# Kernel optimization log

Hardware: AMD Instinct MI355X
Metric: run time of the kernel (lower is better)

The kernel has to match this reference:

```python
import jax, jax.numpy as jnp
import numpy as np

TEMPERATURE = 1.0
EPS = 1e-12  # matches torch F.normalize default eps


def setup_inputs() -> dict:
    key = jax.random.key(0)
    k1, k2 = jax.random.split(key)
    B, N, D = 8, 2048, 768
    final_features = jax.random.normal(k1, (B, N, D), dtype=jnp.float32)
    mid_features = jax.random.normal(k2, (B, N, D), dtype=jnp.float32)
    return {"final_features": final_features, "mid_features": mid_features}


def reference(final_features, mid_features):
    B, N, D = final_features.shape
    dtype = final_features.dtype

    mid = mid_features.astype(jnp.float32)
    # L2-normalize along feature dim (torch F.normalize: x / max(||x||, eps))
    norm = jnp.maximum(jnp.linalg.norm(mid, axis=-1, keepdims=True), EPS)
    mid_n = mid / norm

    # [B, N, N] cosine similarity
    sim = jnp.einsum("bnd,bmd->bnm", mid_n, mid_n)
    # zero out diagonal (add_self_similarity=False): sim * (1 - eye)
    eye = jnp.eye(N, dtype=sim.dtype)
    sim = sim * (1.0 - eye)[None, :, :]

    # confidence = row-wise max of (zeroed-diagonal) similarity
    confidence = jnp.max(sim, axis=-1)  # [B, N]

    # softmax over scaled similarities (diagonal entries are exactly 0, kept in softmax)
    weights = jax.nn.softmax(sim / TEMPERATURE, axis=-1)  # [B, N, N]

    refined = jnp.einsum("bnm,bmd->bnd", weights, final_features.astype(jnp.float32))

    cw = confidence[..., None].astype(dtype)  # [B, N, 1]
    calibrated = cw * refined.astype(dtype) + (1.0 - cw) * final_features
    return calibrated
```

## Files before the change

kernel.cpp:

```cpp
#include <hip/hip_runtime.h>
#include <hip/hip_bf16.h>

static constexpr int BB = 8;
static constexpr int NN = 2048;
static constexpr int DD = 768;

typedef __attribute__((ext_vector_type(8))) __bf16 bf16x8;
typedef __attribute__((ext_vector_type(4))) float f32x4;

__device__ __forceinline__ void gload_lds16(const __hip_bfloat16* g, __hip_bfloat16* l) {
  __builtin_amdgcn_global_load_lds(
      (const __attribute__((address_space(1))) void*)g,
      (__attribute__((address_space(3))) void*)l,
      16, 0, 0);
}

static constexpr int NORM_BLOCKS = (BB * NN) / 4;
static constexpr int TRANS_BLOCKS = (DD / 32) * (NN / 32) * BB;
__global__ void prep_kernel(const float* __restrict__ mid, __hip_bfloat16* __restrict__ Qn,
                            float* __restrict__ lsum, float* __restrict__ conf,
                            const float* __restrict__ F, __hip_bfloat16* __restrict__ Vt) {
  __shared__ __hip_bfloat16 tile[32][33];
  const int t = threadIdx.x;
  if (blockIdx.x < NORM_BLOCKS) {
    const int wave = t >> 6;
    const int lane = t & 63;
    const size_t row = (size_t)blockIdx.x * 4 + wave;
    if (lane == 0) { lsum[row] = 0.f; conf[row] = 0.f; }
    const float* src = mid + row * DD;

    float4 v[3];
    float ss = 0.f;
#pragma unroll
    for (int j = 0; j < 3; ++j) {
      v[j] = *(const float4*)(src + j * 256 + lane * 4);
      ss += v[j].x * v[j].x + v[j].y * v[j].y + v[j].z * v[j].z + v[j].w * v[j].w;
    }
#pragma unroll
    for (int o = 32; o; o >>= 1) ss += __shfl_xor(ss, o, 64);
    const float inv = 1.0f / fmaxf(sqrtf(ss), 1e-12f);

    __hip_bfloat16* dst = Qn + row * DD;
#pragma unroll
    for (int j = 0; j < 3; ++j) {
      union { ushort4 u; __hip_bfloat16 h[4]; } pk;
      pk.h[0] = __float2bfloat16(v[j].x * inv);
      pk.h[1] = __float2bfloat16(v[j].y * inv);
      pk.h[2] = __float2bfloat16(v[j].z * inv);
      pk.h[3] = __float2bfloat16(v[j].w * inv);
      *(ushort4*)(dst + j * 256 + lane * 4) = pk.u;
    }
  } else {
    const int bid = blockIdx.x - NORM_BLOCKS;
    const int bx = bid % 24;
    const int rest = bid / 24;
    const int by = rest & 63;
    const int b = rest >> 6;
    const int n0 = by * 32;
    const int d0 = bx * 32;
    const int tx = t & 31, ty = t >> 5;
#pragma unroll
    for (int i = 0; i < 4; ++i) {
      const int n = n0 + ty + i * 8;
      tile[ty + i * 8][tx] = __float2bfloat16(F[((size_t)b * NN + n) * DD + d0 + tx]);
    }
    __syncthreads();
#pragma unroll
    for (int i = 0; i < 4; ++i) {
      const int d = d0 + ty + i * 8;
      Vt[((size_t)b * DD + d) * NN + n0 + tx] = tile[tx][ty + i * 8];
    }
  }
}

__global__ __launch_bounds__(256) void gemm_qk_kernel(
    const __hip_bfloat16* __restrict__ Qn,
    __hip_bfloat16* __restrict__ P,
    float* __restrict__ lsum,
    unsigned* __restrict__ conf) {
  __shared__ __hip_bfloat16 smem[4 * 128 * 64];

  const int d = blockIdx.x;
  const int b = d & 7;
  int rem = d >> 3;
  int ti = 0;
  while (rem >= 16 - ti) { rem -= 16 - ti; ++ti; }
  const int tj = ti + rem;
  const int rowBase = ti * 128;
  const int colBase = tj * 128;
  const bool offdiag = (ti != tj);

  const int t = threadIdx.x;
  const int lane = t & 63;
  const int wave = t >> 6;
  const int wRow = wave >> 1;
  const int wCol = wave & 1;
  const int quad = lane >> 4;
  const int l16 = lane & 15;

  const __hip_bfloat16* Abase = Qn + ((size_t)b * NN + rowBase) * DD;
  const __hip_bfloat16* Bbase = Qn + ((size_t)b * NN + colBase) * DD;

  int srow[4], scol[4], sc8[4];
#pragma unroll
  for (int i = 0; i < 4; ++i) {
    const int c = i * 256 + t;
    srow[i] = c >> 3;
    const int col8 = (c & 7) ^ ((c >> 3) & 7);
    scol[i] = col8 * 8;
    sc8[i] = c * 8;
  }

  f32x4 acc[4][4];
#pragma unroll
  for (int i = 0; i < 4; ++i)
#pragma unroll
    for (int j = 0; j < 4; ++j) acc[i][j] = (f32x4){0.f, 0.f, 0.f, 0.f};

  {
    __hip_bfloat16* As = smem;
    __hip_bfloat16* Bs = smem + 128 * 64;
#pragma unroll
    for (int i = 0; i < 4; ++i) {
      gload_lds16(Abase + (size_t)srow[i] * DD + scol[i], As + sc8[i]);
      gload_lds16(Bbase + (size_t)srow[i] * DD + scol[i], Bs + sc8[i]);
    }
  }

  constexpr int NK = DD / 64;
  for (int kk = 0; kk < NK; ++kk) {
    const int cur = kk & 1;
    __syncthreads();
    if (kk + 1 < NK) {
      __hip_bfloat16* As = smem + (1 - cur) * 2 * 128 * 64;
      __hip_bfloat16* Bs = As + 128 * 64;
      const int k0 = (kk + 1) * 64;
#pragma unroll
      for (int i = 0; i < 4; ++i) {
        gload_lds16(Abase + (size_t)srow[i] * DD + (k0 + scol[i]), As + sc8[i]);
        gload_lds16(Bbase + (size_t)srow[i] * DD + (k0 + scol[i]), Bs + sc8[i]);
      }
    }
    const __hip_bfloat16* As = smem + cur * 2 * 128 * 64;
    const __hip_bfloat16* Bs = As + 128 * 64;
#pragma unroll
    for (int ks = 0; ks < 2; ++ks) {
      bf16x8 af[4], bfr[4];
#pragma unroll
      for (int i = 0; i < 4; ++i) {
        const int rA = wRow * 64 + i * 16 + l16;
        const int rB = wCol * 64 + i * 16 + l16;
        const int pA = (ks * 4 + quad) ^ (rA & 7);
        const int pB = (ks * 4 + quad) ^ (rB & 7);
        af[i]  = *(const bf16x8*)(As + rA * 64 + pA * 8);
        bfr[i] = *(const bf16x8*)(Bs + rB * 64 + pB * 8);
      }
#pragma unroll
      for (int mi = 0; mi < 4; ++mi)
#pragma unroll
        for (int ni = 0; ni < 4; ++ni)
          acc[mi][ni] = __builtin_amdgcn_mfma_f32_16x16x32_bf16(af[mi], bfr[ni], acc[mi][ni], 0, 0, 0);
    }
  }

  __syncthreads();
  __hip_bfloat16* Pt = smem;
  __hip_bfloat16* Mt = smem + 128 * 128;

  float csum[4] = {0.f, 0.f, 0.f, 0.f};
  float cmax[4] = {0.f, 0.f, 0.f, 0.f};

#pragma unroll
  for (int mi = 0; mi < 4; ++mi) {
    const int rbase = wRow * 64 + mi * 16 + quad * 4;
    float rs[4] = {0.f, 0.f, 0.f, 0.f};
    float rm[4] = {0.f, 0.f, 0.f, 0.f};
#pragma unroll
    for (int ni = 0; ni < 4; ++ni) {
      const int colL = wCol * 64 + ni * 16 + l16;
      const int col_g = colBase + colL;
      union { ushort4 u; __hip_bfloat16 h[4]; } pk;
#pragma unroll
      for (int r = 0; r < 4; ++r) {
        const int rowL = rbase + r;
        float s = acc[mi][ni][r];
        if (rowBase + rowL == col_g) s = 0.f;
        const float p = __expf(s);
        rm[r] = fmaxf(rm[r], s);
        rs[r] += p;
        csum[ni] += p;
        cmax[ni] = fmaxf(cmax[ni], s);
        pk.h[r] = __float2bfloat16(p);
        Pt[rowL * 128 + (((colL >> 3) ^ (rowL & 7)) << 3) + (colL & 7)] = pk.h[r];
      }
      if (offdiag) {
        *(ushort4*)(Mt + colL * 128 + (((rbase >> 3) ^ (colL & 7)) << 3) + (rbase & 7)) = pk.u;
      }
    }
#pragma unroll
    for (int r = 0; r < 4; ++r) {
      float ps = rs[r], mx = rm[r];
#pragma unroll
      for (int o = 1; o < 16; o <<= 1) {
        ps += __shfl_xor(ps, o, 64);
        mx = fmaxf(mx, __shfl_xor(mx, o, 64));
      }
      if (l16 == 0) {
        const int row_g = rowBase + rbase + r;
        atomicAdd(lsum + (size_t)b * NN + row_g, ps);
        atomicMax(conf + (size_t)b * NN + row_g, __float_as_uint(mx));
      }
    }
  }

  if (offdiag) {
#pragma unroll
    for (int ni = 0; ni < 4; ++ni) {
      float cs = csum[ni];
      float cm = cmax[ni];
      cs += __shfl_xor(cs, 16, 64); cm = fmaxf(cm, __shfl_xor(cm, 16, 64));
      cs += __shfl_xor(cs, 32, 64); cm = fmaxf(cm, __shfl_xor(cm, 32, 64));
      if (quad == 0) {
        const int col_g = colBase + wCol * 64 + ni * 16 + l16;
        atomicAdd(lsum + (size_t)b * NN + col_g, cs);
        atomicMax(conf + (size_t)b * NN + col_g, __float_as_uint(cm));
      }
    }
  }

  __syncthreads();
  {
    const size_t pBase = ((size_t)b * NN + rowBase) * (size_t)NN + colBase;
#pragma unroll
    for (int i = 0; i < 8; ++i) {
      const int c = i * 256 + t;
      const int row = c >> 4;
      const int ck = c & 15;
      *(uint4*)(P + pBase + (size_t)row * NN + ck * 8) =
          *(const uint4*)(Pt + row * 128 + ((ck ^ (row & 7)) << 3));
    }
  }
  if (offdiag) {
    const size_t pBase = ((size_t)b * NN + colBase) * (size_t)NN + rowBase;
#pragma unroll
    for (int i = 0; i < 8; ++i) {
      const int c = i * 256 + t;
      const int row = c >> 4;
      const int ck = c & 15;
      *(uint4*)(P + pBase + (size_t)row * NN + ck * 8) =
          *(const uint4*)(Mt + row * 128 + ((ck ^ (row & 7)) << 3));
    }
  }
}

__global__ __launch_bounds__(256) void gemm_pv_kernel(
    const __hip_bfloat16* __restrict__ P,
    const __hip_bfloat16* __restrict__ Vt,
    const float* __restrict__ lsum,
    const float* __restrict__ conf,
    const float* __restrict__ F,
    float* __restrict__ Out) {
  __shared__ __hip_bfloat16 smem[4 * 128 * 64];

  const int d = blockIdx.x;
  const int work = (d & 7) * 96 + (d >> 3);
  const int colBase = (work % 6) * 128;
  const int rowBase = ((work / 6) & 15) * 128;
  const int b = work / 96;

  const int t = threadIdx.x;
  const int lane = t & 63;
  const int wave = t >> 6;
  const int wRow = wave >> 1;
  const int wCol = wave & 1;
  const int quad = lane >> 4;
  const int l16 = lane & 15;

  const __hip_bfloat16* Abase = P + (size_t)b * NN * NN + (size_t)rowBase * NN;
  const __hip_bfloat16* Bbase = Vt + (size_t)b * DD * NN + (size_t)colBase * NN;

  int srow[4], scol[4], sc8[4];
#pragma unroll
  for (int i = 0; i < 4; ++i) {
    const int c = i * 256 + t;
    srow[i] = c >> 3;
    const int col8 = (c & 7) ^ ((c >> 3) & 7);
    scol[i] = col8 * 8;
    sc8[i] = c * 8;
  }

  f32x4 acc[4][4];
#pragma unroll
  for (int i = 0; i < 4; ++i)
#pragma unroll
    for (int j = 0; j < 4; ++j) acc[i][j] = (f32x4){0.f, 0.f, 0.f, 0.f};

  {
    __hip_bfloat16* As = smem;
    __hip_bfloat16* Bs = smem + 128 * 64;
#pragma unroll
    for (int i = 0; i < 4; ++i) {
      gload_lds16(Abase + (size_t)srow[i] * NN + scol[i], As + sc8[i]);
      gload_lds16(Bbase + (size_t)srow[i] * NN + scol[i], Bs + sc8[i]);
    }
  }

  constexpr int NK = NN / 64;
  for (int kk = 0; kk < NK; ++kk) {
    const int cur = kk & 1;
    __syncthreads();
    if (kk + 1 < NK) {
      __hip_bfloat16* As = smem + (1 - cur) * 2 * 128 * 64;
      __hip_bfloat16* Bs = As + 128 * 64;
      const int k0 = (kk + 1) * 64;
#pragma unroll
      for (int i = 0; i < 4; ++i) {
        gload_lds16(Abase + (size_t)srow[i] * NN + (k0 + scol[i]), As + sc8[i]);
        gload_lds16(Bbase + (size_t)srow[i] * NN + (k0 + scol[i]), Bs + sc8[i]);
      }
    }
    const __hip_bfloat16* As = smem + cur * 2 * 128 * 64;
    const __hip_bfloat16* Bs = As + 128 * 64;
#pragma unroll
    for (int ks = 0; ks < 2; ++ks) {
      bf16x8 af[4], bfr[4];
#pragma unroll
      for (int i = 0; i < 4; ++i) {
        const int rA = wRow * 64 + i * 16 + l16;
        const int rB = wCol * 64 + i * 16 + l16;
        const int pA = (ks * 4 + quad) ^ (rA & 7);
        const int pB = (ks * 4 + quad) ^ (rB & 7);
        af[i]  = *(const bf16x8*)(As + rA * 64 + pA * 8);
        bfr[i] = *(const bf16x8*)(Bs + rB * 64 + pB * 8);
      }
#pragma unroll
      for (int mi = 0; mi < 4; ++mi)
#pragma unroll
        for (int ni = 0; ni < 4; ++ni)
          acc[mi][ni] = __builtin_amdgcn_mfma_f32_16x16x32_bf16(af[mi], bfr[ni], acc[mi][ni], 0, 0, 0);
    }
  }

#pragma unroll
  for (int mi = 0; mi < 4; ++mi) {
#pragma unroll
    for (int r = 0; r < 4; ++r) {
      const int row_g = rowBase + wRow * 64 + mi * 16 + quad * 4 + r;
      const float li = lsum[(size_t)b * NN + row_g];
      const float cw = conf[(size_t)b * NN + row_g];
      const float inv = 1.0f / li;
      const float* frow = F + ((size_t)b * NN + row_g) * DD;
      float* orow = Out + ((size_t)b * NN + row_g) * DD;
#pragma unroll
      for (int ni = 0; ni < 4; ++ni) {
        const int col_g = colBase + wCol * 64 + ni * 16 + l16;
        const float o = acc[mi][ni][r] * inv;
        orow[col_g] = cw * o + (1.f - cw) * frow[col_g];
      }
    }
  }
}

extern "C" void kernel_launch(void* const* d_in, const int* in_sizes, int n_in,
                              void* d_out, int out_size, void* d_ws, size_t ws_size,
                              hipStream_t stream) {
  const float* F = (const float*)d_in[0];
  const float* M = (const float*)d_in[1];
  float* Out = (float*)d_out;

  char* ws = (char*)d_ws;
  __hip_bfloat16* Qn = (__hip_bfloat16*)(ws);
  __hip_bfloat16* Vt = (__hip_bfloat16*)(ws + 25165824);
  __hip_bfloat16* P  = (__hip_bfloat16*)(ws + 50331648);
  float* lsum        = (float*)(ws + 117440512);
  float* conf        = (float*)(ws + 117506048);

  prep_kernel<<<NORM_BLOCKS + TRANS_BLOCKS, 256, 0, stream>>>(M, Qn, lsum, conf, F, Vt);
  gemm_qk_kernel<<<8 * 136, 256, 0, stream>>>(Qn, P, lsum, (unsigned*)conf);
  gemm_pv_kernel<<<768, 256, 0, stream>>>(P, Vt, lsum, conf, F, Out);
}
```

Before: 266.5 us.

## Move V transpose into QK launch, reorder tiles, widen PV tiles to 128x192

The F-to-bf16 transpose into Vt moves out of the prep kernel and into the QK GEMM launch as extra tail blocks, so it runs alongside the GEMM tiles instead of before them. QK tile enumeration now schedules the off-diagonal tiles first and the diagonal tiles last. The PV GEMM uses 128x192 output tiles with 6 MFMA columns per wave, giving 512 blocks instead of 768. The wider tile cuts redundant re-reads of P but uses more LDS and accumulator registers, which may lower occupancy.

```diff
diff --git a/kernel.cpp b/kernel.cpp
--- a/kernel.cpp
+++ b/kernel.cpp
@@ -17,41 +17,53 @@
 
 static constexpr int NORM_BLOCKS = (BB * NN) / 4;
 static constexpr int TRANS_BLOCKS = (DD / 32) * (NN / 32) * BB;
+static constexpr int QK_BLOCKS = BB * 136;
+
 __global__ void prep_kernel(const float* __restrict__ mid, __hip_bfloat16* __restrict__ Qn,
-                            float* __restrict__ lsum, float* __restrict__ conf,
-                            const float* __restrict__ F, __hip_bfloat16* __restrict__ Vt) {
-  __shared__ __hip_bfloat16 tile[32][33];
+                            float* __restrict__ lsum, float* __restrict__ conf) {
   const int t = threadIdx.x;
-  if (blockIdx.x < NORM_BLOCKS) {
-    const int wave = t >> 6;
-    const int lane = t & 63;
-    const size_t row = (size_t)blockIdx.x * 4 + wave;
-    if (lane == 0) { lsum[row] = 0.f; conf[row] = 0.f; }
-    const float* src = mid + row * DD;
-
-    float4 v[3];
-    float ss = 0.f;
-#pragma unroll
-    for (int j = 0; j < 3; ++j) {
-      v[j] = *(const float4*)(src + j * 256 + lane * 4);
-      ss += v[j].x * v[j].x + v[j].y * v[j].y + v[j].z * v[j].z + v[j].w * v[j].w;
-    }
-#pragma unroll
-    for (int o = 32; o; o >>= 1) ss += __shfl_xor(ss, o, 64);
-    const float inv = 1.0f / fmaxf(sqrtf(ss), 1e-12f);
-
-    __hip_bfloat16* dst = Qn + row * DD;
-#pragma unroll
-    for (int j = 0; j < 3; ++j) {
-      union { ushort4 u; __hip_bfloat16 h[4]; } pk;
-      pk.h[0] = __float2bfloat16(v[j].x * inv);
-      pk.h[1] = __float2bfloat16(v[j].y * inv);
-      pk.h[2] = __float2bfloat16(v[j].z * inv);
-      pk.h[3] = __float2bfloat16(v[j].w * inv);
-      *(ushort4*)(dst + j * 256 + lane * 4) = pk.u;
-    }
-  } else {
-    const int bid = blockIdx.x - NORM_BLOCKS;
+  const int wave = t >> 6;
+  const int lane = t & 63;
+  const size_t row = (size_t)blockIdx.x * 4 + wave;
+  if (lane == 0) { lsum[row] = 0.f; conf[row] = 0.f; }
+  const float* src = mid + row * DD;
+
+  float4 v[3];
+  float ss = 0.f;
+#pragma unroll
+  for (int j = 0; j < 3; ++j) {
+    v[j] = *(const float4*)(src + j * 256 + lane * 4);
+    ss += v[j].x * v[j].x + v[j].y * v[j].y + v[j].z * v[j].z + v[j].w * v[j].w;
+  }
+#pragma unroll
+  for (int o = 32; o; o >>= 1) ss += __shfl_xor(ss, o, 64);
+  const float inv = 1.0f / fmaxf(sqrtf(ss), 1e-12f);
+
+  __hip_bfloat16* dst = Qn + row * DD;
+#pragma unroll
+  for (int j = 0; j < 3; ++j) {
+    union { ushort4 u; __hip_bfloat16 h[4]; } pk;
+    pk.h[0] = __float2bfloat16(v[j].x * inv);
+    pk.h[1] = __float2bfloat16(v[j].y * inv);
+    pk.h[2] = __float2bfloat16(v[j].z * inv);
+    pk.h[3] = __float2bfloat16(v[j].w * inv);
+    *(ushort4*)(dst + j * 256 + lane * 4) = pk.u;
+  }
+}
+
+__global__ __launch_bounds__(256) void gemm_qk_kernel(
+    const __hip_bfloat16* __restrict__ Qn,
+    __hip_bfloat16* __restrict__ P,
+    float* __restrict__ lsum,
+    unsigned* __restrict__ conf,
+    const float* __restrict__ F,
+    __hip_bfloat16* __restrict__ Vt) {
+  __shared__ __hip_bfloat16 smem[4 * 128 * 64];
+  const int t = threadIdx.x;
+
+  if (blockIdx.x >= QK_BLOCKS) {
+    __hip_bfloat16 (*tile)[33] = reinterpret_cast<__hip_bfloat16(*)[33]>(smem);
+    const int bid = blockIdx.x - QK_BLOCKS;
     const int bx = bid % 24;
     const int rest = bid / 24;
     const int by = rest & 63;
@@ -70,27 +82,24 @@
       const int d = d0 + ty + i * 8;
       Vt[((size_t)b * DD + d) * NN + n0 + tx] = tile[tx][ty + i * 8];
     }
-  }
-}
-
-__global__ __launch_bounds__(256) void gemm_qk_kernel(
-    const __hip_bfloat16* __restrict__ Qn,
-    __hip_bfloat16* __restrict__ P,
-    float* __restrict__ lsum,
-    unsigned* __restrict__ conf) {
-  __shared__ __hip_bfloat16 smem[4 * 128 * 64];
+    return;
+  }
 
   const int d = blockIdx.x;
   const int b = d & 7;
   int rem = d >> 3;
-  int ti = 0;
-  while (rem >= 16 - ti) { rem -= 16 - ti; ++ti; }
-  const int tj = ti + rem;
+  int ti, tj;
+  if (rem < 120) {
+    ti = 0;
+    while (rem >= 15 - ti) { rem -= 15 - ti; ++ti; }
+    tj = ti + 1 + rem;
+  } else {
+    ti = tj = rem - 120;
+  }
   const int rowBase = ti * 128;
   const int colBase = tj * 128;
   const bool offdiag = (ti != tj);
 
-  const int t = threadIdx.x;
   const int lane = t & 63;
   const int wave = t >> 6;
   const int wRow = wave >> 1;
@@ -260,13 +269,14 @@
     const float* __restrict__ conf,
     const float* __restrict__ F,
     float* __restrict__ Out) {
-  __shared__ __hip_bfloat16 smem[4 * 128 * 64];
+  __shared__ __hip_bfloat16 smem[2 * (128 * 64 + 192 * 64)];
 
   const int d = blockIdx.x;
-  const int work = (d & 7) * 96 + (d >> 3);
-  const int colBase = (work % 6) * 128;
-  const int rowBase = ((work / 6) & 15) * 128;
-  const int b = work / 96;
+  const int work = (d & 7) * 64 + (d >> 3);
+  const int b = work >> 6;
+  const int w6 = work & 63;
+  const int colBase = (w6 & 3) * 192;
+  const int rowBase = (w6 >> 2) * 128;
 
   const int t = threadIdx.x;
   const int lane = t & 63;
@@ -279,30 +289,41 @@
   const __hip_bfloat16* Abase = P + (size_t)b * NN * NN + (size_t)rowBase * NN;
   const __hip_bfloat16* Bbase = Vt + (size_t)b * DD * NN + (size_t)colBase * NN;
 
-  int srow[4], scol[4], sc8[4];
+  int srowA[4], scolA[4], sc8A[4];
 #pragma unroll
   for (int i = 0; i < 4; ++i) {
     const int c = i * 256 + t;
-    srow[i] = c >> 3;
-    const int col8 = (c & 7) ^ ((c >> 3) & 7);
-    scol[i] = col8 * 8;
-    sc8[i] = c * 8;
-  }
-
-  f32x4 acc[4][4];
+    srowA[i] = c >> 3;
+    scolA[i] = ((c & 7) ^ ((c >> 3) & 7)) * 8;
+    sc8A[i] = c * 8;
+  }
+  int srowB[6], scolB[6], sc8B[6];
+#pragma unroll
+  for (int i = 0; i < 6; ++i) {
+    const int c = i * 256 + t;
+    srowB[i] = c >> 3;
+    scolB[i] = ((c & 7) ^ ((c >> 3) & 7)) * 8;
+    sc8B[i] = c * 8;
+  }
+
+  f32x4 acc[4][6];
 #pragma unroll
   for (int i = 0; i < 4; ++i)
 #pragma unroll
-    for (int j = 0; j < 4; ++j) acc[i][j] = (f32x4){0.f, 0.f, 0.f, 0.f};
+    for (int j = 0; j < 6; ++j) acc[i][j] = (f32x4){0.f, 0.f, 0.f, 0.f};
+
+  constexpr int ABUF = 128 * 64;
+  constexpr int BUFSTRIDE = 128 * 64 + 192 * 64;
 
   {
     __hip_bfloat16* As = smem;
-    __hip_bfloat16* Bs = smem + 128 * 64;
-#pragma unroll
-    for (int i = 0; i < 4; ++i) {
-      gload_lds16(Abase + (size_t)srow[i] * NN + scol[i], As + sc8[i]);
-      gload_lds16(Bbase + (size_t)srow[i] * NN + scol[i], Bs + sc8[i]);
-    }
+    __hip_bfloat16* Bs = smem + ABUF;
+#pragma unroll
+    for (int i = 0; i < 4; ++i)
+      gload_lds16(Abase + (size_t)srowA[i] * NN + scolA[i], As + sc8A[i]);
+#pragma unroll
+    for (int i = 0; i < 6; ++i)
+      gload_lds16(Bbase + (size_t)srowB[i] * NN + scolB[i], Bs + sc8B[i]);
   }
 
   constexpr int NK = NN / 64;
@@ -310,33 +331,37 @@
     const int cur = kk & 1;
     __syncthreads();
     if (kk + 1 < NK) {
-      __hip_bfloat16* As = smem + (1 - cur) * 2 * 128 * 64;
-      __hip_bfloat16* Bs = As + 128 * 64;
+      __hip_bfloat16* As = smem + (1 - cur) * BUFSTRIDE;
+      __hip_bfloat16* Bs = As + ABUF;
       const int k0 = (kk + 1) * 64;
 #pragma unroll
-      for (int i = 0; i < 4; ++i) {
-        gload_lds16(Abase + (size_t)srow[i] * NN + (k0 + scol[i]), As + sc8[i]);
-        gload_lds16(Bbase + (size_t)srow[i] * NN + (k0 + scol[i]), Bs + sc8[i]);
-      }
-    }
-    const __hip_bfloat16* As = smem + cur * 2 * 128 * 64;
-    const __hip_bfloat16* Bs = As + 128 * 64;
+      for (int i = 0; i < 4; ++i)
+        gload_lds16(Abase + (size_t)srowA[i] * NN + (k0 + scolA[i]), As + sc8A[i]);
+#pragma unroll
+      for (int i = 0; i < 6; ++i)
+        gload_lds16(Bbase + (size_t)srowB[i] * NN + (k0 + scolB[i]), Bs + sc8B[i]);
+    }
+    const __hip_bfloat16* As = smem + cur * BUFSTRIDE;
+    const __hip_bfloat16* Bs = As + ABUF;
 #pragma unroll
     for (int ks = 0; ks < 2; ++ks) {
-      bf16x8 af[4], bfr[4];
+      bf16x8 af[4], bfr[6];
 #pragma unroll
       for (int i = 0; i < 4; ++i) {
         const int rA = wRow * 64 + i * 16 + l16;
-        const int rB = wCol * 64 + i * 16 + l16;
         const int pA = (ks * 4 + quad) ^ (rA & 7);
+        af[i] = *(const bf16x8*)(As + rA * 64 + pA * 8);
+      }
+#pragma unroll
+      for (int i = 0; i < 6; ++i) {
+        const int rB = wCol * 96 + i * 16 + l16;
         const int pB = (ks * 4 + quad) ^ (rB & 7);
-        af[i]  = *(const bf16x8*)(As + rA * 64 + pA * 8);
         bfr[i] = *(const bf16x8*)(Bs + rB * 64 + pB * 8);
       }
 #pragma unroll
       for (int mi = 0; mi < 4; ++mi)
 #pragma unroll
-        for (int ni = 0; ni < 4; ++ni)
+        for (int ni = 0; ni < 6; ++ni)
           acc[mi][ni] = __builtin_amdgcn_mfma_f32_16x16x32_bf16(af[mi], bfr[ni], acc[mi][ni], 0, 0, 0);
     }
   }
@@ -352,8 +377,8 @@
       const float* frow = F + ((size_t)b * NN + row_g) * DD;
       float* orow = Out + ((size_t)b * NN + row_g) * DD;
 #pragma unroll
-      for (int ni = 0; ni < 4; ++ni) {
-        const int col_g = colBase + wCol * 64 + ni * 16 + l16;
+      for (int ni = 0; ni < 6; ++ni) {
+        const int col_g = colBase + wCol * 96 + ni * 16 + l16;
         const float o = acc[mi][ni][r] * inv;
         orow[col_g] = cw * o + (1.f - cw) * frow[col_g];
       }
@@ -375,7 +400,7 @@
   float* lsum        = (float*)(ws + 117440512);
   float* conf        = (float*)(ws + 117506048);
 
-  prep_kernel<<<NORM_BLOCKS + TRANS_BLOCKS, 256, 0, stream>>>(M, Qn, lsum, conf, F, Vt);
-  gemm_qk_kernel<<<8 * 136, 256, 0, stream>>>(Qn, P, lsum, (unsigned*)conf);
-  gemm_pv_kernel<<<768, 256, 0, stream>>>(P, Vt, lsum, conf, F, Out);
+  prep_kernel<<<NORM_BLOCKS, 256, 0, stream>>>(M, Qn, lsum, conf);
+  gemm_qk_kernel<<<QK_BLOCKS + TRANS_BLOCKS, 256, 0, stream>>>(Qn, P, lsum, (unsigned*)conf, F, Vt);
+  gemm_pv_kernel<<<512, 256, 0, stream>>>(P, Vt, lsum, conf, F, Out);
 }
```

New measurement: 258.8 us. -2.9%, faster.
